# Kernel tuning notes

Hardware: AMD Instinct MI355X
Metric: run time of the kernel (lower is better)

Reference implementation:

```python
import jax, jax.numpy as jnp
import numpy as np
from jax import lax

TAU = 2.0      # LIF membrane time constant
V_TH = 1.0     # firing threshold, hard reset to 0
SG_SLOPE = 4.0 # surrogate-gradient sigmoid slope

@jax.custom_vjp
def spike(u):
    return (u >= 0.0).astype(u.dtype)

def _spike_fwd(u):
    return spike(u), u

def _spike_bwd(u, g):
    s = jax.nn.sigmoid(SG_SLOPE * u)
    return (g * SG_SLOPE * s * (1.0 - s),)

spike.defvjp(_spike_fwd, _spike_bwd)

def lif(x):
    """LIF neuron over leading time dim. x: [T, ...] -> spikes [T, ...]."""
    def step(v, xt):
        v = v + (xt - v) / TAU          # leaky integrate
        s = spike(v - V_TH)             # fire
        v = v * (1.0 - s)               # hard reset
        return v, s
    _, spikes = lax.scan(step, jnp.zeros_like(x[0]), x)
    return spikes

def linear(x, W, b):
    return x @ W + b

def ssa(x_q, x_kv, Wq, bq, Wk, bk, Wv, bv, Wo, bo, n_heads, alpha):
    """Spiking Self-Attention (Spikformer-style): no softmax, scale=alpha."""
    T, B, N, D = x_q.shape
    M = x_kv.shape[2]
    d = D // n_heads
    q = lif(linear(x_q, Wq, bq)).reshape(T, B, N, n_heads, d).transpose(0, 1, 3, 2, 4)
    k = lif(linear(x_kv, Wk, bk)).reshape(T, B, M, n_heads, d).transpose(0, 1, 3, 2, 4)
    v = lif(linear(x_kv, Wv, bv)).reshape(T, B, M, n_heads, d).transpose(0, 1, 3, 2, 4)
    attn = jnp.einsum('tbhnd,tbhmd->tbhnm', q, k)          # spiking score matrix
    out = jnp.einsum('tbhnm,tbhmd->tbhnd', attn, v) * alpha
    out = lif(out)                                          # attention LIF
    out = out.transpose(0, 1, 3, 2, 4).reshape(T, B, N, D)
    return lif(linear(out, Wo, bo))                         # projection + LIF

def spiking_mlp(x, W1, b1, W2, b2):
    h = lif(linear(x, W1, b1))
    return lif(linear(h, W2, b2))

def setup_inputs() -> dict:
    key = jax.random.key(0)
    T, B, N, D, F = 4, 4, 512, 512, 2048
    ks = jax.random.split(key, 16)
    sc = 1.0 / np.sqrt(D)
    def w(k, shape, s):
        return jax.random.normal(k, shape, dtype=jnp.float32) * s
    return {
        'x': jax.random.normal(ks[0], (T, B, N, D), dtype=jnp.float32),
        'enc_output': jax.random.normal(ks[1], (T, B, N, D), dtype=jnp.float32),
        # self-attention params
        'Wq_s': w(ks[2], (D, D), sc), 'bq_s': jnp.zeros((D,), jnp.float32),
        'Wk_s': w(ks[3], (D, D), sc), 'bk_s': jnp.zeros((D,), jnp.float32),
        'Wv_s': w(ks[4], (D, D), sc), 'bv_s': jnp.zeros((D,), jnp.float32),
        'Wo_s': w(ks[5], (D, D), sc), 'bo_s': jnp.zeros((D,), jnp.float32),
        # cross-attention params
        'Wq_c': w(ks[6], (D, D), sc), 'bq_c': jnp.zeros((D,), jnp.float32),
        'Wk_c': w(ks[7], (D, D), sc), 'bk_c': jnp.zeros((D,), jnp.float32),
        'Wv_c': w(ks[8], (D, D), sc), 'bv_c': jnp.zeros((D,), jnp.float32),
        'Wo_c': w(ks[9], (D, D), sc), 'bo_c': jnp.zeros((D,), jnp.float32),
        # MLP params
        'W1': w(ks[10], (D, F), sc), 'b1': jnp.zeros((F,), jnp.float32),
        'W2': w(ks[11], (F, D), 1.0 / np.sqrt(F)), 'b2': jnp.zeros((D,), jnp.float32),
    }

def reference(x, enc_output,
              Wq_s, bq_s, Wk_s, bk_s, Wv_s, bv_s, Wo_s, bo_s,
              Wq_c, bq_c, Wk_c, bk_c, Wv_c, bv_c, Wo_c, bo_c,
              W1, b1, W2, b2):
    n_heads, alpha = 8, 0.125
    x = x + ssa(x, x, Wq_s, bq_s, Wk_s, bk_s, Wv_s, bv_s, Wo_s, bo_s, n_heads, alpha)
    x = x + ssa(x, enc_output, Wq_c, bq_c, Wk_c, bk_c, Wv_c, bv_c, Wo_c, bo_c, n_heads, alpha)
    x = x + spiking_mlp(x, W1, b1, W2, b2)
    return x
```

## Files before the change

kernel.cpp:

```cpp
#include <hip/hip_runtime.h>
#include <cstddef>

#define T_STEPS 4
#define BN 2048
#define N_TOK 512
#define D_DIM 512
#define F_DIM 2048

#define MODE_SPK 0
#define MODE_SPK_ADD 1
#define MODE_OUT 2

#define FLAG_CAP (2u * 1024u * 1024u)

typedef float f32x4 __attribute__((ext_vector_type(4)));
typedef short s16x8 __attribute__((ext_vector_type(8)));
typedef unsigned int u32;

__device__ __forceinline__ float bf2f(unsigned short u) {
  unsigned int x = ((unsigned int)u) << 16;
  float f;
  __builtin_memcpy(&f, &x, 4);
  return f;
}
__device__ __forceinline__ unsigned short f2bf(float f) {
  unsigned int x;
  __builtin_memcpy(&x, &f, 4);
  x += 0x7fffu + ((x >> 16) & 1u);
  return (unsigned short)(x >> 16);
}

__global__ __launch_bounds__(256) void wsplit_k(
    const float* w0, const float* w1, const float* w2, const float* w3,
    const float* w4, const float* w5, const float* w6, const float* w7,
    const float* w8, const float* w9,
    unsigned short* __restrict__ WhT, unsigned short* __restrict__ WmT) {
  __shared__ float T[32][33];
  const int tile = blockIdx.x;
  const float* w;
  int Kd, Nd, lt;
  size_t off;
  if (tile < 2048) {
    const float* ws[8] = {w0, w1, w2, w3, w4, w5, w6, w7};
    int m = tile >> 8;
    lt = tile & 255; Kd = 512; Nd = 512; off = (size_t)m * 262144; w = ws[m];
  } else if (tile < 3072) {
    lt = tile - 2048; Kd = 512; Nd = 2048; off = 2097152; w = w8;
  } else {
    lt = tile - 3072; Kd = 2048; Nd = 512; off = 3145728; w = w9;
  }
  const int tilesK = Kd / 32;
  const int tk = lt % tilesK, tn = lt / tilesK;
  {
    int r = threadIdx.x >> 3, c4 = (threadIdx.x & 7) * 4;
    float4 v = *reinterpret_cast<const float4*>(
        w + (size_t)(tk * 32 + r) * Nd + tn * 32 + c4);
    T[r][c4 + 0] = v.x; T[r][c4 + 1] = v.y;
    T[r][c4 + 2] = v.z; T[r][c4 + 3] = v.w;
  }
  __syncthreads();
  {
    int n = threadIdx.x >> 3, k4 = (threadIdx.x & 7) * 4;
    float wv[4];
#pragma unroll
    for (int j = 0; j < 4; ++j) wv[j] = T[k4 + j][n];
    size_t ob = off + (size_t)(tn * 32 + n) * Kd + tk * 32 + k4;
    ushort4 h, m2;
    unsigned short* hp = &h.x; unsigned short* mp = &m2.x;
#pragma unroll
    for (int j = 0; j < 4; ++j) {
      unsigned short hh = f2bf(wv[j]);
      float r = wv[j] - bf2f(hh);
      hp[j] = hh; mp[j] = f2bf(r);
    }
    *reinterpret_cast<ushort4*>(WhT + ob) = h;
    *reinterpret_cast<ushort4*>(WmT + ob) = m2;
  }
}

__global__ void zero_k(unsigned int* c) {
  if (threadIdx.x < 8) c[threadIdx.x] = 0u;
}

__global__ __launch_bounds__(256) void asplit_k(
    const float* __restrict__ A1, const unsigned short* __restrict__ A2,
    unsigned short* __restrict__ Ah, unsigned short* __restrict__ Am) {
  const size_t base = ((size_t)blockIdx.x * 256 + threadIdx.x) * 8;
  float4 f0 = *reinterpret_cast<const float4*>(A1 + base);
  float4 f1 = *reinterpret_cast<const float4*>(A1 + base + 4);
  float av[8] = {f0.x, f0.y, f0.z, f0.w, f1.x, f1.y, f1.z, f1.w};
  if (A2 != nullptr) {
    uint4 s = *reinterpret_cast<const uint4*>(A2 + base);
    const unsigned int* pu = &s.x;
#pragma unroll
    for (int j = 0; j < 4; ++j) {
      av[2 * j]     += bf2f((unsigned short)(pu[j] & 0xffffu));
      av[2 * j + 1] += bf2f((unsigned short)(pu[j] >> 16));
    }
  }
  unsigned int ph[4], pm[4];
#pragma unroll
  for (int j = 0; j < 4; ++j) {
    unsigned short h0 = f2bf(av[2 * j]);
    unsigned short h1 = f2bf(av[2 * j + 1]);
    float r0 = av[2 * j] - bf2f(h0);
    float r1 = av[2 * j + 1] - bf2f(h1);
    ph[j] = (unsigned int)h0 | ((unsigned int)h1 << 16);
    pm[j] = (unsigned int)f2bf(r0) | ((unsigned int)f2bf(r1) << 16);
  }
  uint4 vh; vh.x = ph[0]; vh.y = ph[1]; vh.z = ph[2]; vh.w = ph[3];
  uint4 vm; vm.x = pm[0]; vm.y = pm[1]; vm.z = pm[2]; vm.w = pm[3];
  *reinterpret_cast<uint4*>(Ah + base) = vh;
  *reinterpret_cast<uint4*>(Am + base) = vm;
}

__global__ __launch_bounds__(256, 4) void gemm_ns(
    const unsigned short* __restrict__ Ah, const unsigned short* __restrict__ Am,
    const unsigned short* __restrict__ WhTa, const unsigned short* __restrict__ WhTb,
    const unsigned short* __restrict__ WhTc,
    const unsigned short* __restrict__ WmTa, const unsigned short* __restrict__ WmTb,
    const unsigned short* __restrict__ WmTc,
    const float* __restrict__ ba, const float* __restrict__ bb,
    const float* __restrict__ bc,
    const unsigned short* Sprev, const float* __restrict__ Xres,
    const unsigned short* __restrict__ S12,
    void* outa, void* outb, void* outc,
    unsigned int* __restrict__ cnt, unsigned int* __restrict__ flags,
    int N, int K, int nxb, int mode, float errC) {
  __shared__ char smem[36864];

  const int sel = (int)blockIdx.x / nxb;
  const int nb = (int)blockIdx.x - sel * nxb;
  const unsigned short* WhT = sel == 0 ? WhTa : (sel == 1 ? WhTb : WhTc);
  const unsigned short* WmT = sel == 0 ? WmTa : (sel == 1 ? WmTb : WmTc);
  const float* bias = sel == 0 ? ba : (sel == 1 ? bb : bc);
  void* outv = sel == 0 ? outa : (sel == 1 ? outb : outc);
  const bool hasAm = (Am != nullptr);

  const int tid = threadIdx.x;
  const int lane = tid & 63;
  const int wave = tid >> 6;
  const int wr = wave >> 1, wcq = wave & 1;
  const int lm = lane & 15, quad = lane >> 4;
  const int n0 = nb * 64;
  const int bn0 = (int)blockIdx.y * 16;

  const int srow = tid >> 2;
  const int skg = tid & 3;
  const size_t aoff_row = (size_t)((srow >> 4) * BN + bn0 + (srow & 15)) * K;
  const size_t boff_row = (size_t)(n0 + srow) * K;

  f32x4 accH[2][2], accM[2][2], accA[2][2];
#pragma unroll
  for (int i = 0; i < 2; ++i)
#pragma unroll
    for (int j = 0; j < 2; ++j) {
      accH[i][j] = (f32x4){0.f, 0.f, 0.f, 0.f};
      accM[i][j] = (f32x4){0.f, 0.f, 0.f, 0.f};
      accA[i][j] = (f32x4){0.f, 0.f, 0.f, 0.f};
    }

  uint4 pah0 = {0,0,0,0}, pah1 = {0,0,0,0};
  uint4 pam0 = {0,0,0,0}, pam1 = {0,0,0,0};
  uint4 pwh0, pwh1, pwm0, pwm1;

#define LOAD_TILE(K0)                                                          \
  do {                                                                         \
    pah0 = *reinterpret_cast<const uint4*>(Ah + aoff_row + (K0) + skg * 8);    \
    pah1 = *reinterpret_cast<const uint4*>(Ah + aoff_row + (K0) + 32 + skg * 8);\
    if (hasAm) {                                                               \
      pam0 = *reinterpret_cast<const uint4*>(Am + aoff_row + (K0) + skg * 8);  \
      pam1 = *reinterpret_cast<const uint4*>(Am + aoff_row + (K0) + 32 + skg * 8);\
    }                                                                          \
    pwh0 = *reinterpret_cast<const uint4*>(WhT + boff_row + (K0) + skg * 8);   \
    pwh1 = *reinterpret_cast<const uint4*>(WhT + boff_row + (K0) + 32 + skg * 8);\
    pwm0 = *reinterpret_cast<const uint4*>(WmT + boff_row + (K0) + skg * 8);   \
    pwm1 = *reinterpret_cast<const uint4*>(WmT + boff_row + (K0) + 32 + skg * 8);\
  } while (0)

#define STAGE()                                                                \
  do {                                                                         \
    char* p = smem + srow * 144 + skg * 16;                                    \
    *reinterpret_cast<uint4*>(p + 0) = pah0;                                   \
    *reinterpret_cast<uint4*>(p + 64) = pah1;                                  \
    if (hasAm) {                                                               \
      *reinterpret_cast<uint4*>(p + 9216) = pam0;                              \
      *reinterpret_cast<uint4*>(p + 9216 + 64) = pam1;                         \
    }                                                                          \
    *reinterpret_cast<uint4*>(p + 18432) = pwh0;                               \
    *reinterpret_cast<uint4*>(p + 18432 + 64) = pwh1;                          \
    *reinterpret_cast<uint4*>(p + 27648) = pwm0;                               \
    *reinterpret_cast<uint4*>(p + 27648 + 64) = pwm1;                          \
  } while (0)

  const int aoff0 = (wr * 32 + lm) * 144 + quad * 16;
  const int aoff1 = aoff0 + 16 * 144;
  const int boff0 = (wcq * 32 + lm) * 144 + quad * 16;
  const int boff1 = boff0 + 16 * 144;

  LOAD_TILE(0);
  for (int k0 = 0; k0 < K; k0 += 64) {
    STAGE();
    __syncthreads();
    if (k0 + 64 < K) LOAD_TILE(k0 + 64);
#pragma unroll
    for (int kk = 0; kk < 2; ++kk) {
      const int kb = kk * 64;
      s16x8 aH0 = *reinterpret_cast<const s16x8*>(smem + 0 + aoff0 + kb);
      s16x8 aH1 = *reinterpret_cast<const s16x8*>(smem + 0 + aoff1 + kb);
      s16x8 bH0 = *reinterpret_cast<const s16x8*>(smem + 18432 + boff0 + kb);
      s16x8 bH1 = *reinterpret_cast<const s16x8*>(smem + 18432 + boff1 + kb);
      s16x8 bM0 = *reinterpret_cast<const s16x8*>(smem + 27648 + boff0 + kb);
      s16x8 bM1 = *reinterpret_cast<const s16x8*>(smem + 27648 + boff1 + kb);
      s16x8 aA0 = aH0 & (short)0x7FFF;
      s16x8 aA1 = aH1 & (short)0x7FFF;
      s16x8 bA0 = bH0 & (short)0x7FFF;
      s16x8 bA1 = bH1 & (short)0x7FFF;
      accH[0][0] = __builtin_amdgcn_mfma_f32_16x16x32_bf16(aH0, bH0, accH[0][0], 0, 0, 0);
      accH[0][1] = __builtin_amdgcn_mfma_f32_16x16x32_bf16(aH0, bH1, accH[0][1], 0, 0, 0);
      accH[1][0] = __builtin_amdgcn_mfma_f32_16x16x32_bf16(aH1, bH0, accH[1][0], 0, 0, 0);
      accH[1][1] = __builtin_amdgcn_mfma_f32_16x16x32_bf16(aH1, bH1, accH[1][1], 0, 0, 0);
      accM[0][0] = __builtin_amdgcn_mfma_f32_16x16x32_bf16(aH0, bM0, accM[0][0], 0, 0, 0);
      accM[0][1] = __builtin_amdgcn_mfma_f32_16x16x32_bf16(aH0, bM1, accM[0][1], 0, 0, 0);
      accM[1][0] = __builtin_amdgcn_mfma_f32_16x16x32_bf16(aH1, bM0, accM[1][0], 0, 0, 0);
      accM[1][1] = __builtin_amdgcn_mfma_f32_16x16x32_bf16(aH1, bM1, accM[1][1], 0, 0, 0);
      if (hasAm) {
        s16x8 aM0 = *reinterpret_cast<const s16x8*>(smem + 9216 + aoff0 + kb);
        s16x8 aM1 = *reinterpret_cast<const s16x8*>(smem + 9216 + aoff1 + kb);
        accM[0][0] = __builtin_amdgcn_mfma_f32_16x16x32_bf16(aM0, bH0, accM[0][0], 0, 0, 0);
        accM[0][1] = __builtin_amdgcn_mfma_f32_16x16x32_bf16(aM0, bH1, accM[0][1], 0, 0, 0);
        accM[1][0] = __builtin_amdgcn_mfma_f32_16x16x32_bf16(aM1, bH0, accM[1][0], 0, 0, 0);
        accM[1][1] = __builtin_amdgcn_mfma_f32_16x16x32_bf16(aM1, bH1, accM[1][1], 0, 0, 0);
      }
      accA[0][0] = __builtin_amdgcn_mfma_f32_16x16x32_bf16(aA0, bA0, accA[0][0], 0, 0, 0);
      accA[0][1] = __builtin_amdgcn_mfma_f32_16x16x32_bf16(aA0, bA1, accA[0][1], 0, 0, 0);
      accA[1][0] = __builtin_amdgcn_mfma_f32_16x16x32_bf16(aA1, bA0, accA[1][0], 0, 0, 0);
      accA[1][1] = __builtin_amdgcn_mfma_f32_16x16x32_bf16(aA1, bA1, accA[1][1], 0, 0, 0);
    }
    __syncthreads();
  }
#undef LOAD_TILE
#undef STAGE

  float* UXS = (float*)smem;
  float* UXA = (float*)(smem + 8192);
  if (wr == 1) {
#pragma unroll
    for (int mt = 0; mt < 2; ++mt)
#pragma unroll
      for (int nt = 0; nt < 2; ++nt)
#pragma unroll
        for (int j = 0; j < 4; ++j) {
          int i = mt * 8 + nt * 4 + j;
          UXS[i * 128 + wcq * 64 + lane] = accH[mt][nt][j] + accM[mt][nt][j];
          UXA[i * 128 + wcq * 64 + lane] = accA[mt][nt][j];
        }
  }
  __syncthreads();
  if (wr == 0) {
#pragma unroll
    for (int nt = 0; nt < 2; ++nt) {
      const int col = n0 + wcq * 32 + nt * 16 + lm;
      const double bb2 = (double)bias[col];
#pragma unroll
      for (int j = 0; j < 4; ++j) {
        const int bn = bn0 + quad * 4 + j;
        float sv[4], Ev[4];
        sv[0] = accH[0][nt][j] + accM[0][nt][j];
        sv[1] = accH[1][nt][j] + accM[1][nt][j];
        sv[2] = UXS[(0 * 8 + nt * 4 + j) * 128 + wcq * 64 + lane];
        sv[3] = UXS[(1 * 8 + nt * 4 + j) * 128 + wcq * 64 + lane];
        Ev[0] = errC * accA[0][nt][j];
        Ev[1] = errC * accA[1][nt][j];
        Ev[2] = errC * UXA[(0 * 8 + nt * 4 + j) * 128 + wcq * 64 + lane];
        Ev[3] = errC * UXA[(1 * 8 + nt * 4 + j) * 128 + wcq * 64 + lane];
        double v = 0.0;
        float errv = 0.f;
        bool flg = false;
        unsigned int spbits = 0;
#pragma unroll
        for (int t = 0; t < T_STEPS; ++t) {
          double u = (double)sv[t] + bb2;
          v = v + (u - v) * 0.5;
          errv = (errv + Ev[t]) * 0.5f;
          if (fabs(v - 1.0) < 2.0 * (double)errv + 1e-9) flg = true;
          float s = (v >= 1.0) ? 1.0f : 0.0f;
          if (v >= 1.0) { v = 0.0; errv = 0.f; }
          size_t idx = (size_t)(t * BN + bn) * N + col;
          if (mode == MODE_SPK) {
            ((unsigned short*)outv)[idx] = f2bf(s);
          } else if (mode == MODE_SPK_ADD) {
            float sp = bf2f(Sprev[idx]);
            if (sp != 0.f) spbits |= (1u << t);
            ((unsigned short*)outv)[idx] = f2bf(s + sp);
          } else {
            ((float*)outv)[idx] =
                (float)((double)Xres[idx] + (double)bf2f(S12[idx]) + (double)s);
          }
        }
        if (flg) {
          unsigned int rec = (unsigned int)(bn * N + col) |
                             ((unsigned int)sel << 22) | (spbits << 24);
          unsigned int ix = atomicAdd(cnt, 1u);
          if (ix < FLAG_CAP) flags[ix] = rec;
        }
      }
    }
  }
}

__global__ __launch_bounds__(256) void fix_k(
    const void* __restrict__ A1v, const unsigned short* __restrict__ A2,
    const float* __restrict__ Wa, const float* __restrict__ Wb,
    const float* __restrict__ Wc,
    const float* __restrict__ ba, const float* __restrict__ bb,
    const float* __restrict__ bc,
    const float* __restrict__ Xres, const unsigned short* __restrict__ S12,
    void* outa, void* outb, void* outc,
    const unsigned int* __restrict__ cnt, const unsigned int* __restrict__ flags,
    int N, int K, int mode, int a1bf) {
  unsigned int count = *cnt;
  if (count > FLAG_CAP) count = FLAG_CAP;
  const int lane = threadIdx.x & 63;
  const unsigned int wgid = blockIdx.x * 4 + (threadIdx.x >> 6);
  const unsigned int nw = gridDim.x * 4;
  for (unsigned int i = wgid; i < count; i += nw) {
    unsigned int rec = flags[i];
    int idxn = (int)(rec & 0x3FFFFFu);
    int sel = (int)((rec >> 22) & 3u);
    unsigned int spb = rec >> 24;
    int bn = idxn / N;
    int col = idxn - bn * N;
    const float* W = sel == 0 ? Wa : (sel == 1 ? Wb : Wc);
    const float* bias = sel == 0 ? ba : (sel == 1 ? bb : bc);
    void* outv = sel == 0 ? outa : (sel == 1 ? outb : outc);
    double acc0 = 0, acc1 = 0, acc2 = 0, acc3 = 0;
    for (int k = lane; k < K; k += 64) {
      double w = (double)W[(size_t)k * N + col];
      double a0, a1, a2, a3;
      if (a1bf) {
        const unsigned short* A1 = (const unsigned short*)A1v;
        a0 = (double)bf2f(A1[(size_t)(0 * BN + bn) * K + k]);
        a1 = (double)bf2f(A1[(size_t)(1 * BN + bn) * K + k]);
        a2 = (double)bf2f(A1[(size_t)(2 * BN + bn) * K + k]);
        a3 = (double)bf2f(A1[(size_t)(3 * BN + bn) * K + k]);
      } else {
        const float* A1 = (const float*)A1v;
        a0 = (double)A1[(size_t)(0 * BN + bn) * K + k];
        a1 = (double)A1[(size_t)(1 * BN + bn) * K + k];
        a2 = (double)A1[(size_t)(2 * BN + bn) * K + k];
        a3 = (double)A1[(size_t)(3 * BN + bn) * K + k];
      }
      if (A2 != nullptr) {
        a0 += (double)bf2f(A2[(size_t)(0 * BN + bn) * K + k]);
        a1 += (double)bf2f(A2[(size_t)(1 * BN + bn) * K + k]);
        a2 += (double)bf2f(A2[(size_t)(2 * BN + bn) * K + k]);
        a3 += (double)bf2f(A2[(size_t)(3 * BN + bn) * K + k]);
      }
      acc0 += a0 * w; acc1 += a1 * w; acc2 += a2 * w; acc3 += a3 * w;
    }
#pragma unroll
    for (int off = 32; off >= 1; off >>= 1) {
      acc0 += __shfl_down(acc0, off);
      acc1 += __shfl_down(acc1, off);
      acc2 += __shfl_down(acc2, off);
      acc3 += __shfl_down(acc3, off);
    }
    if (lane == 0) {
      double uu[4] = {acc0, acc1, acc2, acc3};
      double v = 0.0;
#pragma unroll
      for (int t = 0; t < T_STEPS; ++t) {
        double u = uu[t] + (double)bias[col];
        v = v + (u - v) * 0.5;
        float s = (v >= 1.0) ? 1.0f : 0.0f;
        if (v >= 1.0) v = 0.0;
        size_t idx = (size_t)(t * BN + bn) * N + col;
        if (mode == MODE_SPK) {
          ((unsigned short*)outv)[idx] = f2bf(s);
        } else if (mode == MODE_SPK_ADD) {
          ((unsigned short*)outv)[idx] =
              f2bf(s + (((spb >> t) & 1u) ? 1.0f : 0.0f));
        } else {
          ((float*)outv)[idx] =
              (float)((double)Xres[idx] + (double)bf2f(S12[idx]) + (double)s);
        }
      }
    }
  }
}

__global__ __launch_bounds__(256) void attn_k(const unsigned short* __restrict__ Q,
                                              const unsigned short* __restrict__ K,
                                              const unsigned short* __restrict__ V,
                                              float* __restrict__ O) {
  __shared__ char smem[43008];
  const int blk = blockIdx.x;
  const int h = blk & 7;
  const int tb = blk >> 3;
  const size_t base = (size_t)tb * (N_TOK * D_DIM) + h * 64;
  const int tid = threadIdx.x;
  const int lane = tid & 63;
  const int wave = tid >> 6;
  const int lm = lane & 15, quad = lane >> 4;

  f32x4 sacc[4];
#pragma unroll
  for (int ct = 0; ct < 4; ++ct) sacc[ct] = (f32x4){0.f, 0.f, 0.f, 0.f};

  const int dq = wave;
  const int pi = lane;

  uint4 ka0, ka1, kb0, kb1, va0, va1, vb0, vb1;
#define ALOAD(c)                                                              \
  do {                                                                        \
    const unsigned short* kp =                                                \
        K + base + (size_t)((c) * 128 + 2 * pi) * D_DIM + dq * 16;            \
    const unsigned short* vp =                                                \
        V + base + (size_t)((c) * 128 + 2 * pi) * D_DIM + dq * 16;            \
    ka0 = *(const uint4*)(kp);     ka1 = *(const uint4*)(kp + 8);             \
    kb0 = *(const uint4*)(kp + D_DIM); kb1 = *(const uint4*)(kp + D_DIM + 8); \
    va0 = *(const uint4*)(vp);     va1 = *(const uint4*)(vp + 8);             \
    vb0 = *(const uint4*)(vp + D_DIM); vb1 = *(const uint4*)(vp + D_DIM + 8); \
  } while (0)

  ALOAD(0);
  for (int c = 0; c < 4; ++c) {
    __syncthreads();
    {
      u32 kw[8]  = {ka0.x, ka0.y, ka0.z, ka0.w, ka1.x, ka1.y, ka1.z, ka1.w};
      u32 kw2[8] = {kb0.x, kb0.y, kb0.z, kb0.w, kb1.x, kb1.y, kb1.z, kb1.w};
      u32 vw[8]  = {va0.x, va0.y, va0.z, va0.w, va1.x, va1.y, va1.z, va1.w};
      u32 vw2[8] = {vb0.x, vb0.y, vb0.z, vb0.w, vb1.x, vb1.y, vb1.z, vb1.w};
#pragma unroll
      for (int i = 0; i < 16; ++i) {
        u32 kl = (kw[i >> 1] >> ((i & 1) * 16)) & 0xffffu;
        u32 kh = (kw2[i >> 1] >> ((i & 1) * 16)) & 0xffffu;
        *(u32*)(smem + (dq * 16 + i) * 336 + pi * 4) = kl | (kh << 16);
        u32 vl = (vw[i >> 1] >> ((i & 1) * 16)) & 0xffffu;
        u32 vh = (vw2[i >> 1] >> ((i & 1) * 16)) & 0xffffu;
        *(u32*)(smem + 21504 + (dq * 16 + i) * 336 + pi * 4) = vl | (vh << 16);
      }
    }
    __syncthreads();
    if (c < 3) ALOAD(c + 1);
#pragma unroll
    for (int ks = 0; ks < 4; ++ks) {
      s16x8 a = *(const s16x8*)(smem + (wave * 16 + lm) * 336 +
                                (ks * 32 + quad * 8) * 2);
#pragma unroll
      for (int ct = 0; ct < 4; ++ct) {
        s16x8 b = *(const s16x8*)(smem + 21504 + (ct * 16 + lm) * 336 +
                                  (ks * 32 + quad * 8) * 2);
        sacc[ct] = __builtin_amdgcn_mfma_f32_16x16x32_bf16(a, b, sacc[ct], 0, 0, 0);
      }
    }
  }
#undef ALOAD
  __syncthreads();

#pragma unroll
  for (int ct = 0; ct < 4; ++ct) {
    unsigned short sh[4], sm[4];
#pragma unroll
    for (int j = 0; j < 4; ++j) {
      float s = sacc[ct][j];
      unsigned short hh = f2bf(s);
      sh[j] = hh;
      sm[j] = f2bf(s - bf2f(hh));
    }
    u32 shp0 = (u32)sh[0] | ((u32)sh[1] << 16);
    u32 shp1 = (u32)sh[2] | ((u32)sh[3] << 16);
    u32 smp0 = (u32)sm[0] | ((u32)sm[1] << 16);
    u32 smp1 = (u32)sm[2] | ((u32)sm[3] << 16);
    int row = ct * 16 + lm;
    int col = wave * 16 + quad * 4;
    uint2 wh; wh.x = shp0; wh.y = shp1;
    uint2 wm; wm.x = smp0; wm.y = smp1;
    *(uint2*)(smem + row * 176 + col * 2) = wh;
    *(uint2*)(smem + 11264 + row * 176 + col * 2) = wm;
  }
  __syncthreads();

  s16x8 bh[4][2], bm[4][2];
#pragma unroll
  for (int ct = 0; ct < 4; ++ct)
#pragma unroll
    for (int ks = 0; ks < 2; ++ks) {
      bh[ct][ks] = *(const s16x8*)(smem + (ct * 16 + lm) * 176 +
                                   (ks * 32 + quad * 8) * 2);
      bm[ct][ks] = *(const s16x8*)(smem + 11264 + (ct * 16 + lm) * 176 +
                                   (ks * 32 + quad * 8) * 2);
    }
  const int nw = wave * 128;
#pragma unroll
  for (int rt = 0; rt < 8; ++rt) {
    const int n = nw + rt * 16 + lm;
    s16x8 a0 = *(const s16x8*)(Q + base + (size_t)n * D_DIM + quad * 8);
    s16x8 a1 = *(const s16x8*)(Q + base + (size_t)n * D_DIM + 32 + quad * 8);
    f32x4 o[4];
#pragma unroll
    for (int ct = 0; ct < 4; ++ct) o[ct] = (f32x4){0.f, 0.f, 0.f, 0.f};
#pragma unroll
    for (int ct = 0; ct < 4; ++ct) {
      o[ct] = __builtin_amdgcn_mfma_f32_16x16x32_bf16(a0, bh[ct][0], o[ct], 0, 0, 0);
      o[ct] = __builtin_amdgcn_mfma_f32_16x16x32_bf16(a0, bm[ct][0], o[ct], 0, 0, 0);
      o[ct] = __builtin_amdgcn_mfma_f32_16x16x32_bf16(a1, bh[ct][1], o[ct], 0, 0, 0);
      o[ct] = __builtin_amdgcn_mfma_f32_16x16x32_bf16(a1, bm[ct][1], o[ct], 0, 0, 0);
    }
#pragma unroll
    for (int ct = 0; ct < 4; ++ct)
#pragma unroll
      for (int j = 0; j < 4; ++j) {
        int rr = nw + rt * 16 + quad * 4 + j;
        O[base + (size_t)rr * D_DIM + ct * 16 + lm] = o[ct][j] * 0.125f;
      }
  }
}

__global__ __launch_bounds__(256) void lif_plane(const float* __restrict__ U,
                                                 unsigned short* __restrict__ S) {
  int e = blockIdx.x * 256 + threadIdx.x;
  double v = 0.0;
#pragma unroll
  for (int t = 0; t < T_STEPS; ++t) {
    size_t idx = (size_t)t * (BN * D_DIM) + e;
    double u = (double)U[idx];
    v = v + (u - v) * 0.5;
    float s = (v >= 1.0) ? 1.0f : 0.0f;
    v = (v >= 1.0) ? 0.0 : v;
    S[idx] = f2bf(s);
  }
}

extern "C" void kernel_launch(void* const* d_in, const int* in_sizes, int n_in,
                              void* d_out, int out_size, void* d_ws, size_t ws_size,
                              hipStream_t stream) {
  const float* x    = (const float*)d_in[0];
  const float* enc  = (const float*)d_in[1];
  const float* Wq_s = (const float*)d_in[2];
  const float* bq_s = (const float*)d_in[3];
  const float* Wk_s = (const float*)d_in[4];
  const float* bk_s = (const float*)d_in[5];
  const float* Wv_s = (const float*)d_in[6];
  const float* bv_s = (const float*)d_in[7];
  const float* Wo_s = (const float*)d_in[8];
  const float* bo_s = (const float*)d_in[9];
  const float* Wq_c = (const float*)d_in[10];
  const float* bq_c = (const float*)d_in[11];
  const float* Wk_c = (const float*)d_in[12];
  const float* bk_c = (const float*)d_in[13];
  const float* Wv_c = (const float*)d_in[14];
  const float* bv_c = (const float*)d_in[15];
  const float* Wo_c = (const float*)d_in[16];
  const float* bo_c = (const float*)d_in[17];
  const float* W1   = (const float*)d_in[18];
  const float* b1   = (const float*)d_in[19];
  const float* W2   = (const float*)d_in[20];
  const float* b2   = (const float*)d_in[21];
  float* out = (float*)d_out;

  char* pool = (char*)d_ws;
  const size_t MB = 1024 * 1024;
  unsigned short* qs     = (unsigned short*)(pool + 0 * MB);
  unsigned short* ks     = (unsigned short*)(pool + 8 * MB);
  unsigned short* vs     = (unsigned short*)(pool + 16 * MB);
  float*          u_attn = (float*)(pool + 24 * MB);
  unsigned short* as_    = (unsigned short*)(pool + 0 * MB);
  unsigned short* h_spk  = (unsigned short*)(pool + 8 * MB);
  unsigned short* s1     = (unsigned short*)(pool + 40 * MB);
  unsigned short* WhT    = (unsigned short*)(pool + 48 * MB);
  unsigned short* WmT    = (unsigned short*)(pool + 56 * MB);
  unsigned short* Ahp    = (unsigned short*)(pool + 64 * MB);
  unsigned short* Amp    = (unsigned short*)(pool + 72 * MB);
  unsigned int*   flags  = (unsigned int*)(pool + 80 * MB);
  unsigned int*   cnts   = (unsigned int*)(pool + 88 * MB);

  const size_t OQS = 0, OKS = 262144, OVS = 524288, OOS = 786432;
  const size_t OQC = 1048576, OKC = 1310720, OVC = 1572864, OOC = 1835008;
  const size_t OW1 = 2097152, OW2 = 3145728;

  const float ERR512 = 1.1f * 512.f * 5.96e-8f + 4.6e-5f;
  const float ERR2048 = 1.1f * 2048.f * 5.96e-8f + 4.6e-5f;

  const unsigned short* NULS = nullptr;
  const float* NULF = nullptr;
  dim3 blk(256);
  int gLif = (BN * D_DIM) / 256;

  zero_k<<<1, 64, 0, stream>>>(cnts);
  wsplit_k<<<4096, blk, 0, stream>>>(Wq_s, Wk_s, Wv_s, Wo_s, Wq_c, Wk_c, Wv_c,
                                     Wo_c, W1, W2, WhT, WmT);

  asplit_k<<<2048, blk, 0, stream>>>(x, NULS, Ahp, Amp);
  gemm_ns<<<dim3(24, 128), blk, 0, stream>>>(
      Ahp, Amp, WhT + OQS, WhT + OKS, WhT + OVS, WmT + OQS, WmT + OKS, WmT + OVS,
      bq_s, bk_s, bv_s, NULS, NULF, NULS, qs, ks, vs,
      cnts + 0, flags, 512, 512, 8, MODE_SPK, ERR512);
  fix_k<<<1024, blk, 0, stream>>>(x, NULS, Wq_s, Wk_s, Wv_s,
      bq_s, bk_s, bv_s, NULF, NULS, qs, ks, vs, cnts + 0, flags, 512, 512, MODE_SPK, 0);
  attn_k<<<128, blk, 0, stream>>>(qs, ks, vs, u_attn);
  lif_plane<<<gLif, blk, 0, stream>>>(u_attn, as_);
  gemm_ns<<<dim3(8, 128), blk, 0, stream>>>(
      as_, NULS, WhT + OOS, WhT + OOS, WhT + OOS, WmT + OOS, WmT + OOS, WmT + OOS,
      bo_s, bo_s, bo_s, NULS, NULF, NULS, s1, s1, s1,
      cnts + 1, flags, 512, 512, 8, MODE_SPK, ERR512);
  fix_k<<<1024, blk, 0, stream>>>(as_, NULS, Wo_s, Wo_s, Wo_s,
      bo_s, bo_s, bo_s, NULF, NULS, s1, s1, s1, cnts + 1, flags, 512, 512, MODE_SPK, 1);

  asplit_k<<<2048, blk, 0, stream>>>(x, s1, Ahp, Amp);
  gemm_ns<<<dim3(8, 128), blk, 0, stream>>>(
      Ahp, Amp, WhT + OQC, WhT + OQC, WhT + OQC, WmT + OQC, WmT + OQC, WmT + OQC,
      bq_c, bq_c, bq_c, NULS, NULF, NULS, qs, qs, qs,
      cnts + 2, flags, 512, 512, 8, MODE_SPK, ERR512);
  fix_k<<<1024, blk, 0, stream>>>(x, s1, Wq_c, Wq_c, Wq_c,
      bq_c, bq_c, bq_c, NULF, NULS, qs, qs, qs, cnts + 2, flags, 512, 512, MODE_SPK, 0);
  asplit_k<<<2048, blk, 0, stream>>>(enc, NULS, Ahp, Amp);
  gemm_ns<<<dim3(16, 128), blk, 0, stream>>>(
      Ahp, Amp, WhT + OKC, WhT + OVC, WhT + OVC, WmT + OKC, WmT + OVC, WmT + OVC,
      bk_c, bv_c, bv_c, NULS, NULF, NULS, ks, vs, vs,
      cnts + 3, flags, 512, 512, 8, MODE_SPK, ERR512);
  fix_k<<<1024, blk, 0, stream>>>(enc, NULS, Wk_c, Wv_c, Wv_c,
      bk_c, bv_c, bv_c, NULF, NULS, ks, vs, vs, cnts + 3, flags, 512, 512, MODE_SPK, 0);
  attn_k<<<128, blk, 0, stream>>>(qs, ks, vs, u_attn);
  lif_plane<<<gLif, blk, 0, stream>>>(u_attn, as_);
  gemm_ns<<<dim3(8, 128), blk, 0, stream>>>(
      as_, NULS, WhT + OOC, WhT + OOC, WhT + OOC, WmT + OOC, WmT + OOC, WmT + OOC,
      bo_c, bo_c, bo_c, s1, NULF, NULS, s1, s1, s1,
      cnts + 4, flags, 512, 512, 8, MODE_SPK_ADD, ERR512);
  fix_k<<<1024, blk, 0, stream>>>(as_, NULS, Wo_c, Wo_c, Wo_c,
      bo_c, bo_c, bo_c, NULF, NULS, s1, s1, s1, cnts + 4, flags, 512, 512, MODE_SPK_ADD, 1);

  asplit_k<<<2048, blk, 0, stream>>>(x, s1, Ahp, Amp);
  gemm_ns<<<dim3(32, 128), blk, 0, stream>>>(
      Ahp, Amp, WhT + OW1, WhT + OW1, WhT + OW1, WmT + OW1, WmT + OW1, WmT + OW1,
      b1, b1, b1, NULS, NULF, NULS, h_spk, h_spk, h_spk,
      cnts + 5, flags, 2048, 512, 32, MODE_SPK, ERR512);
  fix_k<<<1024, blk, 0, stream>>>(x, s1, W1, W1, W1,
      b1, b1, b1, NULF, NULS, h_spk, h_spk, h_spk, cnts + 5, flags, 2048, 512, MODE_SPK, 0);
  gemm_ns<<<dim3(8, 128), blk, 0, stream>>>(
      h_spk, NULS, WhT + OW2, WhT + OW2, WhT + OW2, WmT + OW2, WmT + OW2, WmT + OW2,
      b2, b2, b2, NULS, x, s1, out, out, out,
      cnts + 6, flags, 512, 2048, 8, MODE_OUT, ERR2048);
  fix_k<<<1024, blk, 0, stream>>>(h_spk, NULS, W2, W2, W2,
      b2, b2, b2, x, s1, out, out, out, cnts + 6, flags, 512, 2048, MODE_OUT, 1);

  (void)in_sizes; (void)n_in; (void)out_size; (void)ws_size;
}
```

Measured before the change: 690.8 us.

## Fuse borderline-spike fp64 fixup into GEMM epilogue via shared-memory flag list

Borderline neurons whose membrane potential lies within the error bound of the threshold are no longer written to a global flag buffer for a separate fix_k launch. Each GEMM block now collects them in a shared-memory list and recomputes them in fp64 after a block barrier. This removes seven fix_k launches, the zero_k launch and the global atomic counter traffic. In exchange every GEMM block carries the fixup tail, which may cause load imbalance where flags cluster, and the shared list has no capacity check.

```diff
diff --git a/kernel.cpp b/kernel.cpp
--- a/kernel.cpp
+++ b/kernel.cpp
@@ -10,8 +10,6 @@
 #define MODE_SPK 0
 #define MODE_SPK_ADD 1
 #define MODE_OUT 2
-
-#define FLAG_CAP (2u * 1024u * 1024u)
 
 typedef float f32x4 __attribute__((ext_vector_type(4)));
 typedef short s16x8 __attribute__((ext_vector_type(8)));
@@ -78,10 +76,6 @@
   }
 }
 
-__global__ void zero_k(unsigned int* c) {
-  if (threadIdx.x < 8) c[threadIdx.x] = 0u;
-}
-
 __global__ __launch_bounds__(256) void asplit_k(
     const float* __restrict__ A1, const unsigned short* __restrict__ A2,
     unsigned short* __restrict__ Ah, unsigned short* __restrict__ Am) {
@@ -122,11 +116,13 @@
     const unsigned short* __restrict__ WmTc,
     const float* __restrict__ ba, const float* __restrict__ bb,
     const float* __restrict__ bc,
+    const void* __restrict__ A1o, const unsigned short* __restrict__ A2o,
+    const float* __restrict__ Woa, const float* __restrict__ Wob,
+    const float* __restrict__ Woc,
     const unsigned short* Sprev, const float* __restrict__ Xres,
     const unsigned short* __restrict__ S12,
     void* outa, void* outb, void* outc,
-    unsigned int* __restrict__ cnt, unsigned int* __restrict__ flags,
-    int N, int K, int nxb, int mode, float errC) {
+    int N, int K, int nxb, int mode, int a1bf, float errC) {
   __shared__ char smem[36864];
 
   const int sel = (int)blockIdx.x / nxb;
@@ -134,6 +130,7 @@
   const unsigned short* WhT = sel == 0 ? WhTa : (sel == 1 ? WhTb : WhTc);
   const unsigned short* WmT = sel == 0 ? WmTa : (sel == 1 ? WmTb : WmTc);
   const float* bias = sel == 0 ? ba : (sel == 1 ? bb : bc);
+  const float* Worig = sel == 0 ? Woa : (sel == 1 ? Wob : Woc);
   void* outv = sel == 0 ? outa : (sel == 1 ? outb : outc);
   const bool hasAm = (Am != nullptr);
 
@@ -244,6 +241,9 @@
 
   float* UXS = (float*)smem;
   float* UXA = (float*)(smem + 8192);
+  u32* nfl = (u32*)(smem + 16384);
+  u32* flst = (u32*)(smem + 16388);
+  if (tid == 0) *nfl = 0u;
   if (wr == 1) {
 #pragma unroll
     for (int mt = 0; mt < 2; ++mt)
@@ -299,63 +299,44 @@
           }
         }
         if (flg) {
-          unsigned int rec = (unsigned int)(bn * N + col) |
-                             ((unsigned int)sel << 22) | (spbits << 24);
-          unsigned int ix = atomicAdd(cnt, 1u);
-          if (ix < FLAG_CAP) flags[ix] = rec;
+          unsigned int rec = (unsigned int)(bn * N + col) | (spbits << 24);
+          unsigned int ix = atomicAdd(nfl, 1u);
+          flst[ix] = rec;
         }
       }
     }
   }
-}
-
-__global__ __launch_bounds__(256) void fix_k(
-    const void* __restrict__ A1v, const unsigned short* __restrict__ A2,
-    const float* __restrict__ Wa, const float* __restrict__ Wb,
-    const float* __restrict__ Wc,
-    const float* __restrict__ ba, const float* __restrict__ bb,
-    const float* __restrict__ bc,
-    const float* __restrict__ Xres, const unsigned short* __restrict__ S12,
-    void* outa, void* outb, void* outc,
-    const unsigned int* __restrict__ cnt, const unsigned int* __restrict__ flags,
-    int N, int K, int mode, int a1bf) {
-  unsigned int count = *cnt;
-  if (count > FLAG_CAP) count = FLAG_CAP;
-  const int lane = threadIdx.x & 63;
-  const unsigned int wgid = blockIdx.x * 4 + (threadIdx.x >> 6);
-  const unsigned int nw = gridDim.x * 4;
-  for (unsigned int i = wgid; i < count; i += nw) {
-    unsigned int rec = flags[i];
-    int idxn = (int)(rec & 0x3FFFFFu);
-    int sel = (int)((rec >> 22) & 3u);
+  __syncthreads();
+
+  const u32 count = *nfl;
+  for (u32 i = (u32)wave; i < count; i += 4u) {
+    unsigned int rec = flst[i];
+    int idxn = (int)(rec & 0xFFFFFFu);
     unsigned int spb = rec >> 24;
     int bn = idxn / N;
     int col = idxn - bn * N;
-    const float* W = sel == 0 ? Wa : (sel == 1 ? Wb : Wc);
-    const float* bias = sel == 0 ? ba : (sel == 1 ? bb : bc);
-    void* outv = sel == 0 ? outa : (sel == 1 ? outb : outc);
     double acc0 = 0, acc1 = 0, acc2 = 0, acc3 = 0;
     for (int k = lane; k < K; k += 64) {
-      double w = (double)W[(size_t)k * N + col];
+      double w = (double)Worig[(size_t)k * N + col];
       double a0, a1, a2, a3;
       if (a1bf) {
-        const unsigned short* A1 = (const unsigned short*)A1v;
+        const unsigned short* A1 = (const unsigned short*)A1o;
         a0 = (double)bf2f(A1[(size_t)(0 * BN + bn) * K + k]);
         a1 = (double)bf2f(A1[(size_t)(1 * BN + bn) * K + k]);
         a2 = (double)bf2f(A1[(size_t)(2 * BN + bn) * K + k]);
         a3 = (double)bf2f(A1[(size_t)(3 * BN + bn) * K + k]);
       } else {
-        const float* A1 = (const float*)A1v;
+        const float* A1 = (const float*)A1o;
         a0 = (double)A1[(size_t)(0 * BN + bn) * K + k];
         a1 = (double)A1[(size_t)(1 * BN + bn) * K + k];
         a2 = (double)A1[(size_t)(2 * BN + bn) * K + k];
         a3 = (double)A1[(size_t)(3 * BN + bn) * K + k];
       }
-      if (A2 != nullptr) {
-        a0 += (double)bf2f(A2[(size_t)(0 * BN + bn) * K + k]);
-        a1 += (double)bf2f(A2[(size_t)(1 * BN + bn) * K + k]);
-        a2 += (double)bf2f(A2[(size_t)(2 * BN + bn) * K + k]);
-        a3 += (double)bf2f(A2[(size_t)(3 * BN + bn) * K + k]);
+      if (A2o != nullptr) {
+        a0 += (double)bf2f(A2o[(size_t)(0 * BN + bn) * K + k]);
+        a1 += (double)bf2f(A2o[(size_t)(1 * BN + bn) * K + k]);
+        a2 += (double)bf2f(A2o[(size_t)(2 * BN + bn) * K + k]);
+        a3 += (double)bf2f(A2o[(size_t)(3 * BN + bn) * K + k]);
       }
       acc0 += a0 * w; acc1 += a1 * w; acc2 += a2 * w; acc3 += a3 * w;
     }
@@ -573,8 +554,6 @@
   unsigned short* WmT    = (unsigned short*)(pool + 56 * MB);
   unsigned short* Ahp    = (unsigned short*)(pool + 64 * MB);
   unsigned short* Amp    = (unsigned short*)(pool + 72 * MB);
-  unsigned int*   flags  = (unsigned int*)(pool + 80 * MB);
-  unsigned int*   cnts   = (unsigned int*)(pool + 88 * MB);
 
   const size_t OQS = 0, OKS = 262144, OVS = 524288, OOS = 786432;
   const size_t OQC = 1048576, OKC = 1310720, OVC = 1572864, OOC = 1835008;
@@ -588,62 +567,54 @@
   dim3 blk(256);
   int gLif = (BN * D_DIM) / 256;
 
-  zero_k<<<1, 64, 0, stream>>>(cnts);
   wsplit_k<<<4096, blk, 0, stream>>>(Wq_s, Wk_s, Wv_s, Wo_s, Wq_c, Wk_c, Wv_c,
                                      Wo_c, W1, W2, WhT, WmT);
 
   asplit_k<<<2048, blk, 0, stream>>>(x, NULS, Ahp, Amp);
   gemm_ns<<<dim3(24, 128), blk, 0, stream>>>(
       Ahp, Amp, WhT + OQS, WhT + OKS, WhT + OVS, WmT + OQS, WmT + OKS, WmT + OVS,
-      bq_s, bk_s, bv_s, NULS, NULF, NULS, qs, ks, vs,
-      cnts + 0, flags, 512, 512, 8, MODE_SPK, ERR512);
-  fix_k<<<1024, blk, 0, stream>>>(x, NULS, Wq_s, Wk_s, Wv_s,
-      bq_s, bk_s, bv_s, NULF, NULS, qs, ks, vs, cnts + 0, flags, 512, 512, MODE_SPK, 0);
+      bq_s, bk_s, bv_s, x, NULS, Wq_s, Wk_s, Wv_s,
+      NULS, NULF, NULS, qs, ks, vs,
+      512, 512, 8, MODE_SPK, 0, ERR512);
   attn_k<<<128, blk, 0, stream>>>(qs, ks, vs, u_attn);
   lif_plane<<<gLif, blk, 0, stream>>>(u_attn, as_);
   gemm_ns<<<dim3(8, 128), blk, 0, stream>>>(
       as_, NULS, WhT + OOS, WhT + OOS, WhT + OOS, WmT + OOS, WmT + OOS, WmT + OOS,
-      bo_s, bo_s, bo_s, NULS, NULF, NULS, s1, s1, s1,
-      cnts + 1, flags, 512, 512, 8, MODE_SPK, ERR512);
-  fix_k<<<1024, blk, 0, stream>>>(as_, NULS, Wo_s, Wo_s, Wo_s,
-      bo_s, bo_s, bo_s, NULF, NULS, s1, s1, s1, cnts + 1, flags, 512, 512, MODE_SPK, 1);
+      bo_s, bo_s, bo_s, as_, NULS, Wo_s, Wo_s, Wo_s,
+      NULS, NULF, NULS, s1, s1, s1,
+      512, 512, 8, MODE_SPK, 1, ERR512);
 
   asplit_k<<<2048, blk, 0, stream>>>(x, s1, Ahp, Amp);
   gemm_ns<<<dim3(8, 128), blk, 0, stream>>>(
       Ahp, Amp, WhT + OQC, WhT + OQC, WhT + OQC, WmT + OQC, WmT + OQC, WmT + OQC,
-      bq_c, bq_c, bq_c, NULS, NULF, NULS, qs, qs, qs,
-      cnts + 2, flags, 512, 512, 8, MODE_SPK, ERR512);
-  fix_k<<<1024, blk, 0, stream>>>(x, s1, Wq_c, Wq_c, Wq_c,
-      bq_c, bq_c, bq_c, NULF, NULS, qs, qs, qs, cnts + 2, flags, 512, 512, MODE_SPK, 0);
+      bq_c, bq_c, bq_c, x, s1, Wq_c, Wq_c, Wq_c,
+      NULS, NULF, NULS, qs, qs, qs,
+      512, 512, 8, MODE_SPK, 0, ERR512);
   asplit_k<<<2048, blk, 0, stream>>>(enc, NULS, Ahp, Amp);
   gemm_ns<<<dim3(16, 128), blk, 0, stream>>>(
       Ahp, Amp, WhT + OKC, WhT + OVC, WhT + OVC, WmT + OKC, WmT + OVC, WmT + OVC,
-      bk_c, bv_c, bv_c, NULS, NULF, NULS, ks, vs, vs,
-      cnts + 3, flags, 512, 512, 8, MODE_SPK, ERR512);
-  fix_k<<<1024, blk, 0, stream>>>(enc, NULS, Wk_c, Wv_c, Wv_c,
-      bk_c, bv_c, bv_c, NULF, NULS, ks, vs, vs, cnts + 3, flags, 512, 512, MODE_SPK, 0);
+      bk_c, bv_c, bv_c, enc, NULS, Wk_c, Wv_c, Wv_c,
+      NULS, NULF, NULS, ks, vs, vs,
+      512, 512, 8, MODE_SPK, 0, ERR512);
   attn_k<<<128, blk, 0, stream>>>(qs, ks, vs, u_attn);
   lif_plane<<<gLif, blk, 0, stream>>>(u_attn, as_);
   gemm_ns<<<dim3(8, 128), blk, 0, stream>>>(
       as_, NULS, WhT + OOC, WhT + OOC, WhT + OOC, WmT + OOC, WmT + OOC, WmT + OOC,
-      bo_c, bo_c, bo_c, s1, NULF, NULS, s1, s1, s1,
-      cnts + 4, flags, 512, 512, 8, MODE_SPK_ADD, ERR512);
-  fix_k<<<1024, blk, 0, stream>>>(as_, NULS, Wo_c, Wo_c, Wo_c,
-      bo_c, bo_c, bo_c, NULF, NULS, s1, s1, s1, cnts + 4, flags, 512, 512, MODE_SPK_ADD, 1);
+      bo_c, bo_c, bo_c, as_, NULS, Wo_c, Wo_c, Wo_c,
+      s1, NULF, NULS, s1, s1, s1,
+      512, 512, 8, MODE_SPK_ADD, 1, ERR512);
 
   asplit_k<<<2048, blk, 0, stream>>>(x, s1, Ahp, Amp);
   gemm_ns<<<dim3(32, 128), blk, 0, stream>>>(
       Ahp, Amp, WhT + OW1, WhT + OW1, WhT + OW1, WmT + OW1, WmT + OW1, WmT + OW1,
-      b1, b1, b1, NULS, NULF, NULS, h_spk, h_spk, h_spk,
-      cnts + 5, flags, 2048, 512, 32, MODE_SPK, ERR512);
-  fix_k<<<1024, blk, 0, stream>>>(x, s1, W1, W1, W1,
-      b1, b1, b1, NULF, NULS, h_spk, h_spk, h_spk, cnts + 5, flags, 2048, 512, MODE_SPK, 0);
+      b1, b1, b1, x, s1, W1, W1, W1,
+      NULS, NULF, NULS, h_spk, h_spk, h_spk,
+      2048, 512, 32, MODE_SPK, 0, ERR512);
   gemm_ns<<<dim3(8, 128), blk, 0, stream>>>(
       h_spk, NULS, WhT + OW2, WhT + OW2, WhT + OW2, WmT + OW2, WmT + OW2, WmT + OW2,
-      b2, b2, b2, NULS, x, s1, out, out, out,
-      cnts + 6, flags, 512, 2048, 8, MODE_OUT, ERR2048);
-  fix_k<<<1024, blk, 0, stream>>>(h_spk, NULS, W2, W2, W2,
-      b2, b2, b2, x, s1, out, out, out, cnts + 6, flags, 512, 2048, MODE_OUT, 1);
+      b2, b2, b2, h_spk, NULS, W2, W2, W2,
+      NULS, x, s1, out, out, out,
+      512, 2048, 8, MODE_OUT, 1, ERR2048);
 
   (void)in_sizes; (void)n_in; (void)out_size; (void)ws_size;
 }
```

Result: no change. 697.5 us (+1.0%).
